# Performance work log

Hardware: AMD Instinct MI355X
Metric: run time of the kernel (lower is better)

## Reference

```python
import jax, jax.numpy as jnp
import numpy as np
from jax import lax

QMAX = 127.0  # symmetric int8 fake-quant levels
EPS = 1e-5    # batchnorm eps


def fq(x):
    """Per-tensor symmetric fake-quant with straight-through estimator.
    Simulates ChopSTE: round/clip to low precision in fwd, identity grad in bwd."""
    s = jnp.maximum(jnp.max(jnp.abs(x)) / QMAX, 1e-8)
    q = jnp.clip(jnp.round(x / s), -QMAX, QMAX) * s
    return x + lax.stop_gradient(q - x)


def conv2d(x, w, b):
    # NCHW input, OIHW kernel, padding=1 (SAME for 3x3)
    y = lax.conv_general_dilated(x, w, window_strides=(1, 1),
                                 padding=((1, 1), (1, 1)),
                                 dimension_numbers=('NCHW', 'OIHW', 'NCHW'))
    return y + b[None, :, None, None]


def maxpool2(x):
    return lax.reduce_window(x, -jnp.inf, lax.max, (1, 1, 2, 2), (1, 1, 2, 2), 'VALID')


def bn(x, g, be, m, v):
    inv = g / jnp.sqrt(v + EPS)  # [C]
    return x * inv[None, :, None, None] + (be - m * inv)[None, :, None, None]


def setup_inputs() -> dict:
    key = jax.random.key(0)
    ks = jax.random.split(key, 17)
    B = 8192
    d = {}
    d['x'] = jax.random.normal(ks[0], (B, 1, 28, 28), jnp.float32)
    d['w1'] = jax.random.normal(ks[1], (16, 1, 3, 3), jnp.float32) * 0.3
    d['b1'] = jax.random.normal(ks[2], (16,), jnp.float32) * 0.1
    d['g1'] = jax.random.uniform(ks[3], (16,), jnp.float32, 0.5, 1.5)
    d['be1'] = jax.random.normal(ks[4], (16,), jnp.float32) * 0.1
    d['m1'] = jax.random.normal(ks[5], (16,), jnp.float32) * 0.1
    d['v1'] = jax.random.uniform(ks[6], (16,), jnp.float32, 0.5, 1.5)
    d['w2'] = jax.random.normal(ks[7], (32, 16, 3, 3), jnp.float32) * 0.1
    d['b2'] = jax.random.normal(ks[8], (32,), jnp.float32) * 0.1
    d['g2'] = jax.random.uniform(ks[9], (32,), jnp.float32, 0.5, 1.5)
    d['be2'] = jax.random.normal(ks[10], (32,), jnp.float32) * 0.1
    d['m2'] = jax.random.normal(ks[11], (32,), jnp.float32) * 0.1
    d['v2'] = jax.random.uniform(ks[12], (32,), jnp.float32, 0.5, 1.5)
    d['fw1'] = jax.random.normal(ks[13], (128, 1568), jnp.float32) * 0.03
    d['fb1'] = jax.random.normal(ks[14], (128,), jnp.float32) * 0.1
    d['fw2'] = jax.random.normal(ks[15], (10, 128), jnp.float32) * 0.1
    d['fb2'] = jax.random.normal(ks[16], (10,), jnp.float32) * 0.1
    return d


def reference(x, w1, b1, g1, be1, m1, v1, w2, b2, g2, be2, m2, v2, fw1, fb1, fw2, fb2):
    # block 1: quantized conv -> quantized relu -> quantized bn -> maxpool
    h = fq(conv2d(x, fq(w1), b1))           # [B,16,28,28]
    h = fq(jax.nn.relu(h))
    h = fq(bn(h, g1, be1, m1, v1))
    h = maxpool2(h)                          # [B,16,14,14]
    # block 2
    h = fq(conv2d(h, fq(w2), b2))           # [B,32,14,14]
    h = fq(jax.nn.relu(h))
    h = fq(bn(h, g2, be2, m2, v2))
    h = maxpool2(h)                          # [B,32,7,7]
    # classifier (dropout is identity at inference)
    h = h.reshape(h.shape[0], -1)            # [B,1568]
    h = fq(h @ fq(fw1).T + fb1)              # [B,128]
    h = fq(jax.nn.relu(h))
    out = fq(h @ fq(fw2).T + fb2)            # [B,10]
    return out
```

## Files before the change

### kernel.cpp

```cpp
#include <hip/hip_runtime.h>
#include <math.h>
#include <limits.h>
#include <stdint.h>

#define QMAXF 127.0f
#define BN_EPS 1e-5f
#define NCOPIES 64

typedef int v4i __attribute__((ext_vector_type(4)));
typedef float f32x4 __attribute__((ext_vector_type(4)));
typedef _Float16 f16x8 __attribute__((ext_vector_type(8)));

__device__ __forceinline__ int f2ord(float f){
    int i = __float_as_int(f);
    return i ^ ((i >> 31) & 0x7fffffff);
}
__device__ __forceinline__ float ord2f(int i){
    return __int_as_float(i ^ ((i >> 31) & 0x7fffffff));
}
__device__ __forceinline__ float scale_from_ord(int om){
    return fmaxf(ord2f(om) / QMAXF, 1e-8f);
}
__device__ __forceinline__ float fq_apply(float x, float s){
    float q = rintf(x / s);
    q = fminf(fmaxf(q, -QMAXF), QMAXF);
    return q * s;
}
__device__ __forceinline__ float quant_k(float x, float s){
    float q = rintf(x / s);
    return fminf(fmaxf(q, -QMAXF), QMAXF);
}
__device__ __forceinline__ _Float16 hpart(uint32_t w){
    return __builtin_bit_cast(_Float16, (unsigned short)(w >> 16));
}
__device__ __forceinline__ _Float16 lpart(uint32_t w){
    return __builtin_bit_cast(_Float16, (unsigned short)(w & 0xffffu));
}

__global__ void k_init_stats(int* s1, int* s2, int* sf, int* so, int* wsmax){
    int t = blockIdx.x*blockDim.x + threadIdx.x;
    if (t < 2048){ int j = t & 31; s1[t] = (j < 16) ? INT_MAX : INT_MIN; }
    else if (t < 6144){ int u = t - 2048; int j = u & 63; s2[u] = (j < 32) ? INT_MAX : INT_MIN; }
    else if (t < 6272){ int u = t - 6144; sf[u] = ((u & 1) == 0) ? INT_MAX : INT_MIN; }
    else if (t < 6400){ int u = t - 6272; so[u] = ((u & 1) == 0) ? INT_MAX : INT_MIN; }
    else if (t < 6404){ wsmax[t - 6400] = INT_MIN; }
}

__global__ __launch_bounds__(256) void k_wscales(
    const float* __restrict__ w1, const float* __restrict__ w2,
    const float* __restrict__ fw1, const float* __restrict__ fw2,
    int* __restrict__ wsmax)
{
    __shared__ float red[256];
    int t = threadIdx.x, blk = blockIdx.x;
    const float* src; int n, base, which;
    if (blk < 64){ src = fw1; base = blk*3136; n = 3136; which = 2; }
    else if (blk == 64){ src = w1;  base = 0; n = 144;  which = 0; }
    else if (blk == 65){ src = w2;  base = 0; n = 4608; which = 1; }
    else { src = fw2; base = 0; n = 1280; which = 3; }
    float m = 0.f;
    for (int i = t; i < n; i += 256) m = fmaxf(m, fabsf(src[base + i]));
    red[t] = m; __syncthreads();
    for (int off = 128; off; off >>= 1){
        if (t < off) red[t] = fmaxf(red[t], red[t+off]);
        __syncthreads();
    }
    if (t == 0) atomicMax(&wsmax[which], f2ord(red[0]));
}

__global__ __launch_bounds__(256) void k_pack_weights(
    const float* __restrict__ w1, const float* __restrict__ w2,
    const float* __restrict__ fw1, const float* __restrict__ fw2,
    const int* __restrict__ wsmax,
    _Float16* __restrict__ wpk1h, int8_t* __restrict__ wpk2,
    int8_t* __restrict__ bpk1, float* __restrict__ qfw2,
    float* __restrict__ wscales)
{
    int blk = blockIdx.x, t = threadIdx.x;
    if (blk < 784){
        float s = scale_from_ord(wsmax[2]);
        int i = blk*256 + t;
        int o = i / 1568, k = i - o*1568;
        int c = k / 49, r = k - c*49;
        int kp = r*32 + c;
        int kchunk = kp >> 6, rem = kp & 63, hi = rem >> 4, j = rem & 15;
        int code = (int)quant_k(fw1[i], s);
        bpk1[(o>>4)*25600 + (kchunk*4 + hi)*256 + (o&15)*16 + j] = (int8_t)code;
    } else if (blk == 784){
        float s0 = scale_from_ord(wsmax[0]), s3 = scale_from_ord(wsmax[3]);
        for (int i = t; i < 512; i += 256){
            int grp = i >> 3, j = i & 7;
            int hi = grp >> 4, col = grp & 15;
            _Float16 val = (_Float16)0.f;
            if (hi < 3 && j < 3)
                val = (_Float16)quant_k(w1[col*9 + hi*3 + j], s0);
            wpk1h[i] = val;
        }
        for (int i = t; i < 1280; i += 256) qfw2[i] = fq_apply(fw2[i], s3);
        for (int i = t; i < 4096; i += 256){
            int o = i >> 5, rem = (i & 31) + 32;
            int hi = rem >> 4, j = rem & 15;
            bpk1[(o>>4)*25600 + (24*4 + hi)*256 + (o&15)*16 + j] = 0;
        }
        if (t < 4) wscales[t] = scale_from_ord(wsmax[t]);
    } else {
        float s1 = scale_from_ord(wsmax[1]);
        for (int i = t; i < 6144; i += 256) wpk2[i] = 0;
        __syncthreads();
        for (int i = t; i < 4608; i += 256){
            int co = i / 144, rr = i - co*144, ci = rr / 9, pix = rr - ci*9;
            wpk2[(co >> 4)*3072 + pix*256 + (co & 15)*16 + ci] = (int8_t)(int)quant_k(w2[i], s1);
        }
    }
}

__global__ __launch_bounds__(256) void k_prep_x(
    const float* __restrict__ x, uint32_t* __restrict__ xp)
{
    int i = blockIdx.x*256 + threadIdx.x;
    int b = i / 900, r = i - b*900;
    int yy = r / 30, xx = r - yy*30;
    float val = 0.f;
    if (yy >= 1 && yy <= 28 && xx >= 1 && xx <= 28)
        val = x[(size_t)b*784 + (yy-1)*28 + (xx-1)];
    _Float16 h  = (_Float16)val;
    _Float16 lo = (_Float16)(val - (float)h);
    xp[i] = ((uint32_t)__builtin_bit_cast(unsigned short, h) << 16)
          |  (uint32_t)__builtin_bit_cast(unsigned short, lo);
}

__device__ __forceinline__ void conv1_frag3(const uint32_t* __restrict__ base, bool valid,
                                            f16x8& ahi, f16x8& alo)
{
    uint32_t w0 = valid ? base[0] : 0u;
    uint32_t w1 = valid ? base[1] : 0u;
    uint32_t w2 = valid ? base[2] : 0u;
    _Float16 z = (_Float16)0.f;
    ahi = (f16x8){hpart(w0), hpart(w1), hpart(w2), z, z, z, z, z};
    alo = (f16x8){lpart(w0), lpart(w1), lpart(w2), z, z, z, z, z};
}

__global__ __launch_bounds__(256) void k_conv1s_mfma(
    const uint32_t* __restrict__ xp, const _Float16* __restrict__ wpk1h,
    const float* __restrict__ b1, const float* __restrict__ wscales,
    int* __restrict__ stats1)
{
    int t = threadIdx.x, l = t & 63, wid = t >> 6;
    int hi = l >> 4, col = l & 15;
    f16x8 bv = *(const f16x8*)(wpk1h + (hi*16 + col)*8);
    float sb = b1[col];
    float s0 = wscales[0];
    int tile0 = blockIdx.x*4 + wid;
    int p0 = tile0*16 + (l & 15);
    int b0 = p0 / 784, r = p0 - b0*784;
    int y = r / 28, xx = r - y*28;
    int rowo = (hi < 3) ? hi : 2;
    bool valid = hi < 3;
    const uint32_t* base = xp + (size_t)b0*900 + (y + rowo)*30 + xx;
    float mn = INFINITY, mx = -INFINITY;
    #pragma unroll 1
    for (int it = 0; it < 64; it++){
        f16x8 ahi, alo;
        conv1_frag3(base, valid, ahi, alo);
        f32x4 acc = {0.f, 0.f, 0.f, 0.f};
        acc = __builtin_amdgcn_mfma_f32_16x16x32_f16(ahi, bv, acc, 0, 0, 0);
        acc = __builtin_amdgcn_mfma_f32_16x16x32_f16(alo, bv, acc, 0, 0, 0);
        #pragma unroll
        for (int rg = 0; rg < 4; rg++){
            mn = fminf(mn, acc[rg]); mx = fmaxf(mx, acc[rg]);
        }
        base += (size_t)128*900;
    }
    mn = fmaf(s0, mn, sb);
    mx = fmaf(s0, mx, sb);
    mn = fminf(mn, __shfl_xor(mn, 16)); mn = fminf(mn, __shfl_xor(mn, 32));
    mx = fmaxf(mx, __shfl_xor(mx, 16)); mx = fmaxf(mx, __shfl_xor(mx, 32));
    if (l < 16){
        int* basep = stats1 + (blockIdx.x & (NCOPIES-1))*32;
        atomicMin(&basep[l],      f2ord(mn));
        atomicMax(&basep[16 + l], f2ord(mx));
    }
}

__global__ __launch_bounds__(256) void k_scales_block(
    const int* __restrict__ stats,
    const float* __restrict__ g, const float* __restrict__ be,
    const float* __restrict__ m, const float* __restrict__ v,
    float* __restrict__ s_out, int8_t* __restrict__ t1buf)
{
    __shared__ float cmn[16], cmx[16], invs[16], dds[16], sss[3];
    int t = threadIdx.x;
    if (t < 32){
        bool ismax = t >= 16; int c = t & 15;
        int acc = ismax ? INT_MIN : INT_MAX;
        for (int i = 0; i < NCOPIES; i++){
            int u = stats[i*32 + t];
            acc = ismax ? max(acc, u) : min(acc, u);
        }
        if (ismax) cmx[c] = ord2f(acc); else cmn[c] = ord2f(acc);
    }
    __syncthreads();
    if (t == 0){
        float am = 0.f;
        for (int c = 0; c < 16; c++) am = fmaxf(am, fmaxf(fabsf(cmn[c]), fabsf(cmx[c])));
        float sA_ = fmaxf(am / QMAXF, 1e-8f);
        float rmax = 0.f;
        float q1x[16], q1n[16];
        for (int c = 0; c < 16; c++){
            q1x[c] = fmaxf(fq_apply(cmx[c], sA_), 0.f);
            q1n[c] = fmaxf(fq_apply(cmn[c], sA_), 0.f);
            rmax = fmaxf(rmax, q1x[c]);
        }
        float sB_ = fmaxf(rmax / QMAXF, 1e-8f);
        float am3 = 0.f;
        for (int c = 0; c < 16; c++){
            float inv = g[c] / sqrtf(v[c] + BN_EPS);
            float dd  = be[c] - m[c]*inv;
            invs[c] = inv; dds[c] = dd;
            float ha = fmaf(fq_apply(q1x[c], sB_), inv, dd);
            float hb = fmaf(fq_apply(q1n[c], sB_), inv, dd);
            am3 = fmaxf(am3, fmaxf(fabsf(ha), fabsf(hb)));
        }
        float sC_ = fmaxf(am3 / QMAXF, 1e-8f);
        sss[0] = sA_; sss[1] = sB_; sss[2] = sC_;
        s_out[0] = sA_; s_out[1] = sB_; s_out[2] = sC_;
    }
    __syncthreads();
    float s1 = sss[0], s2 = sss[1], s3 = sss[2];
    for (int e = t; e < 2048; e += 256){
        int c = e >> 7, idx = e & 127;
        float hh = (float)idx * s1;
        float q2 = quant_k(hh, s2);
        float h2 = q2 * s2;
        float hb = fmaf(h2, invs[c], dds[c]);
        t1buf[e] = (int8_t)(int)quant_k(hb, s3);
    }
}

__global__ __launch_bounds__(256) void k_block1_mfma(
    const uint32_t* __restrict__ xp, const _Float16* __restrict__ wpk1h,
    const float* __restrict__ b1, const float* __restrict__ wscales,
    const float* __restrict__ scales, const int8_t* __restrict__ t1buf,
    int8_t* __restrict__ h1q)
{
    __shared__ int8_t T1l[16*132];
    int t = threadIdx.x, l = t & 63, wid = t >> 6;
    for (int e = t; e < 2048; e += 256)
        T1l[(e >> 7)*132 + (e & 127)] = t1buf[e];
    __syncthreads();
    int hi = l >> 4, col = l & 15;
    f16x8 bv = *(const f16x8*)(wpk1h + (hi*16 + col)*8);
    float sb = b1[col];
    float s0 = wscales[0], s1 = scales[0];
    int tile0 = blockIdx.x*4 + wid;
    int grow = tile0*16 + (l & 15);
    int cell = grow >> 2, sub = grow & 3;
    int b0 = cell / 196, rc = cell - b0*196;
    int py = rc / 14, px = rc - py*14;
    int y = 2*py + (sub >> 1), xx = 2*px + (sub & 1);
    int rowo = (hi < 3) ? hi : 2;
    bool valid = hi < 3;
    const uint32_t* base = xp + (size_t)b0*900 + (y + rowo)*30 + xx;
    const int8_t* T1c = T1l + col*132;
    int8_t* h1o = h1q + (size_t)tile0*64 + l;
    #pragma unroll 1
    for (int it = 0; it < 16; it++){
        f16x8 ahi, alo;
        conv1_frag3(base, valid, ahi, alo);
        f32x4 acc = {0.f, 0.f, 0.f, 0.f};
        acc = __builtin_amdgcn_mfma_f32_16x16x32_f16(ahi, bv, acc, 0, 0, 0);
        acc = __builtin_amdgcn_mfma_f32_16x16x32_f16(alo, bv, acc, 0, 0, 0);
        float pool = fmaxf(fmaxf(acc[0], acc[1]), fmaxf(acc[2], acc[3]));
        float conv = fmaf(s0, pool, sb);
        float q = quant_k(conv, s1);
        int idx = (int)fmaxf(q, 0.f);
        *h1o = T1c[idx];
        base += (size_t)512*900;
        h1o  += (size_t)100352*16;
    }
}

__global__ __launch_bounds__(256) void k_conv2s_mfma(
    const int8_t* __restrict__ h1q, const int8_t* __restrict__ wpk2,
    int* __restrict__ stats2)
{
    __shared__ int smn[32], smx[32];
    int t = threadIdx.x, l = t & 63, wid = t >> 6;
    if (t < 32){ smn[t] = INT_MAX; smx[t] = INT_MIN; }
    __syncthreads();
    int hi = l >> 4;
    v4i bv[6];
    #pragma unroll
    for (int nt = 0; nt < 2; nt++)
        #pragma unroll
        for (int s = 0; s < 3; s++)
            bv[nt*3+s] = *(const v4i*)(wpk2 + nt*3072 + (4*s + hi)*256 + (l&15)*16);
    int tile0 = blockIdx.x*4 + wid;
    int grow = tile0*16 + (l & 15);
    int cell_g = grow >> 2;
    int b0 = cell_g / 49, cell = cell_g - b0*49;
    int sub = grow & 3;
    int qy = cell / 7, qx = cell - qy*7;
    int y = 2*qy + (sub >> 1), x = 2*qx + (sub & 1);
    const int8_t* ip = h1q + (size_t)b0*196*16;
    int toff[3];
    #pragma unroll
    for (int s = 0; s < 3; s++){
        int tap = 4*s + hi;
        toff[s] = -1;
        if (tap < 9){
            int ky = tap / 3, kx = tap - ky*3;
            int yy = y + ky - 1, xc = x + kx - 1;
            if (yy >= 0 && yy < 14 && xc >= 0 && xc < 14)
                toff[s] = (yy*14 + xc)*16;
        }
    }
    int mn0 = INT_MAX, mx0 = INT_MIN, mn1 = INT_MAX, mx1 = INT_MIN;
    #pragma unroll 1
    for (int it = 0; it < 16; it++){
        v4i acc0 = (v4i){0,0,0,0}, acc1 = (v4i){0,0,0,0};
        #pragma unroll
        for (int s = 0; s < 3; s++){
            v4i av = (toff[s] >= 0) ? *(const v4i*)(ip + toff[s]) : (v4i){0,0,0,0};
            acc0 = __builtin_amdgcn_mfma_i32_16x16x64_i8(av, bv[s],     acc0, 0, 0, 0);
            acc1 = __builtin_amdgcn_mfma_i32_16x16x64_i8(av, bv[3 + s], acc1, 0, 0, 0);
        }
        #pragma unroll
        for (int r = 0; r < 4; r++){
            mn0 = min(mn0, acc0[r]); mx0 = max(mx0, acc0[r]);
            mn1 = min(mn1, acc1[r]); mx1 = max(mx1, acc1[r]);
        }
        ip += (size_t)512*196*16;
    }
    mn0 = min(mn0, __shfl_xor(mn0, 16)); mn0 = min(mn0, __shfl_xor(mn0, 32));
    mx0 = max(mx0, __shfl_xor(mx0, 16)); mx0 = max(mx0, __shfl_xor(mx0, 32));
    mn1 = min(mn1, __shfl_xor(mn1, 16)); mn1 = min(mn1, __shfl_xor(mn1, 32));
    mx1 = max(mx1, __shfl_xor(mx1, 16)); mx1 = max(mx1, __shfl_xor(mx1, 32));
    if (l < 16){
        atomicMin(&smn[l], mn0);      atomicMax(&smx[l], mx0);
        atomicMin(&smn[16 + l], mn1); atomicMax(&smx[16 + l], mx1);
    }
    __syncthreads();
    if (t < 32){
        int* basep = stats2 + (blockIdx.x & (NCOPIES-1))*64;
        atomicMin(&basep[t],      smn[t]);
        atomicMax(&basep[t + 32], smx[t]);
    }
}

__global__ __launch_bounds__(256) void k_scales2(
    const int* __restrict__ stats,
    const float* __restrict__ g, const float* __restrict__ be,
    const float* __restrict__ m, const float* __restrict__ v,
    const float* __restrict__ b2,
    const float* __restrict__ scales, const float* __restrict__ wscales,
    float* __restrict__ s_out, int8_t* __restrict__ t2buf)
{
    __shared__ float cmn[32], cmx[32], invs[32], dds[32], sss[3];
    int t = threadIdx.x;
    float S = scales[2] * wscales[1];
    if (t < 64){
        bool ismax = t >= 32; int c = t & 31;
        int acc = ismax ? INT_MIN : INT_MAX;
        for (int i = 0; i < NCOPIES; i++){
            int u = stats[i*64 + t];
            acc = ismax ? max(acc, u) : min(acc, u);
        }
        float val = fmaf(S, (float)acc, b2[c]);
        if (ismax) cmx[c] = val; else cmn[c] = val;
    }
    __syncthreads();
    if (t == 0){
        float am = 0.f;
        for (int c = 0; c < 32; c++) am = fmaxf(am, fmaxf(fabsf(cmn[c]), fabsf(cmx[c])));
        float sA_ = fmaxf(am / QMAXF, 1e-8f);
        float rmax = 0.f;
        float q1x[32], q1n[32];
        for (int c = 0; c < 32; c++){
            q1x[c] = fmaxf(fq_apply(cmx[c], sA_), 0.f);
            q1n[c] = fmaxf(fq_apply(cmn[c], sA_), 0.f);
            rmax = fmaxf(rmax, q1x[c]);
        }
        float sB_ = fmaxf(rmax / QMAXF, 1e-8f);
        float am3 = 0.f;
        for (int c = 0; c < 32; c++){
            float inv = g[c] / sqrtf(v[c] + BN_EPS);
            float dd  = be[c] - m[c]*inv;
            invs[c] = inv; dds[c] = dd;
            float ha = fmaf(fq_apply(q1x[c], sB_), inv, dd);
            float hb = fmaf(fq_apply(q1n[c], sB_), inv, dd);
            am3 = fmaxf(am3, fmaxf(fabsf(ha), fabsf(hb)));
        }
        float sC_ = fmaxf(am3 / QMAXF, 1e-8f);
        sss[0] = sA_; sss[1] = sB_; sss[2] = sC_;
        s_out[0] = sA_; s_out[1] = sB_; s_out[2] = sC_;
    }
    __syncthreads();
    float s4 = sss[0], s5 = sss[1], s6 = sss[2];
    for (int e = t; e < 4096; e += 256){
        int c = e >> 7, idx = e & 127;
        float hh = (float)idx * s4;
        float q5 = quant_k(hh, s5);
        float h2 = q5 * s5;
        float hb = fmaf(h2, invs[c], dds[c]);
        t2buf[e] = (int8_t)(int)quant_k(hb, s6);
    }
}

__global__ __launch_bounds__(256) void k_block2_mfma(
    const int8_t* __restrict__ h1q, const int8_t* __restrict__ wpk2,
    const float* __restrict__ b2, const float* __restrict__ scales,
    const float* __restrict__ wscales, const int8_t* __restrict__ t2buf,
    int8_t* __restrict__ h2q)
{
    __shared__ int8_t T2l[32*132];
    int t = threadIdx.x, l = t & 63, wid = t >> 6;
    for (int e = t; e < 4096; e += 256)
        T2l[(e >> 7)*132 + (e & 127)] = t2buf[e];
    __syncthreads();
    int hi = l >> 4, cl = l & 15;
    float S = scales[2] * wscales[1];
    float s4 = scales[3];
    float sb0 = b2[cl], sb1 = b2[16 + cl];
    const int8_t* T2a = T2l + cl*132;
    const int8_t* T2b = T2l + (16 + cl)*132;
    v4i bv[6];
    #pragma unroll
    for (int nt = 0; nt < 2; nt++)
        #pragma unroll
        for (int s = 0; s < 3; s++)
            bv[nt*3+s] = *(const v4i*)(wpk2 + nt*3072 + (4*s + hi)*256 + cl*16);
    int tile0 = blockIdx.x*4 + wid;
    int grow = tile0*16 + (l & 15);
    int cell_g = grow >> 2;
    int b0 = cell_g / 49, cell = cell_g - b0*49;
    int sub = grow & 3;
    int qy = cell / 7, qx = cell - qy*7;
    int y = 2*qy + (sub >> 1), x = 2*qx + (sub & 1);
    const int8_t* ip = h1q + (size_t)b0*196*16;
    int toff[3];
    #pragma unroll
    for (int s = 0; s < 3; s++){
        int tap = 4*s + hi;
        toff[s] = -1;
        if (tap < 9){
            int ky = tap / 3, kx = tap - ky*3;
            int yy = y + ky - 1, xc = x + kx - 1;
            if (yy >= 0 && yy < 14 && xc >= 0 && xc < 14)
                toff[s] = (yy*14 + xc)*16;
        }
    }
    int8_t* h2o = h2q + (size_t)(tile0*4 + hi)*32 + cl;
    #pragma unroll 1
    for (int it = 0; it < 4; it++){
        v4i acc0 = (v4i){0,0,0,0}, acc1 = (v4i){0,0,0,0};
        #pragma unroll
        for (int s = 0; s < 3; s++){
            v4i av = (toff[s] >= 0) ? *(const v4i*)(ip + toff[s]) : (v4i){0,0,0,0};
            acc0 = __builtin_amdgcn_mfma_i32_16x16x64_i8(av, bv[s],     acc0, 0, 0, 0);
            acc1 = __builtin_amdgcn_mfma_i32_16x16x64_i8(av, bv[3 + s], acc1, 0, 0, 0);
        }
        int pool0 = max(max(acc0[0], acc0[1]), max(acc0[2], acc0[3]));
        int pool1 = max(max(acc1[0], acc1[1]), max(acc1[2], acc1[3]));
        float q0 = quant_k(fmaf(S, (float)pool0, sb0), s4);
        float q1 = quant_k(fmaf(S, (float)pool1, sb1), s4);
        h2o[0]  = T2a[(int)fmaxf(q0, 0.f)];
        h2o[16] = T2b[(int)fmaxf(q1, 0.f)];
        ip  += (size_t)2048*196*16;
        h2o += (size_t)100352*32;
    }
}

__global__ __launch_bounds__(256) void k_fc1(
    const int8_t* __restrict__ h2q, const int8_t* __restrict__ bpk1,
    const float* __restrict__ fb1, const float* __restrict__ scales,
    const float* __restrict__ wscales,
    float* __restrict__ fc1o, int* __restrict__ statsFc)
{
    __shared__ int smn, smx;
    int t = threadIdx.x, l = t & 63, wid = t >> 6;
    if (t == 0){ smn = INT_MAX; smx = INT_MIN; }
    __syncthreads();
    int wave_id = blockIdx.x*4 + wid;
    int mtile = wave_id >> 2;
    int quarter = wave_id & 3;
    int hi = l >> 4, lo = l & 15;
    const int8_t* arow = h2q + (size_t)(mtile*16 + lo)*1568;
    v4i acc[2];
    #pragma unroll
    for (int g = 0; g < 2; g++) acc[g] = (v4i){0,0,0,0};
    #pragma unroll 1
    for (int kc = 0; kc < 25; kc++){
        int koff = kc*64 + hi*16;
        v4i av = (v4i){0,0,0,0};
        if (koff < 1568) av = *(const v4i*)(arow + koff);
        #pragma unroll
        for (int g = 0; g < 2; g++){
            v4i bvv = *(const v4i*)(bpk1 + (quarter*2 + g)*25600 + (kc*4 + hi)*256 + lo*16);
            acc[g] = __builtin_amdgcn_mfma_i32_16x16x64_i8(av, bvv, acc[g], 0, 0, 0);
        }
    }
    float Sfc = scales[5] * wscales[2];
    float lmn = INFINITY, lmx = -INFINITY;
    #pragma unroll
    for (int g = 0; g < 2; g++){
        int o = (quarter*2 + g)*16 + lo;
        float bias = fb1[o];
        #pragma unroll
        for (int r = 0; r < 4; r++){
            int m = mtile*16 + hi*4 + r;
            float val = fmaf(Sfc, (float)acc[g][r], bias);
            fc1o[(size_t)m*128 + o] = val;
            lmn = fminf(lmn, val); lmx = fmaxf(lmx, val);
        }
    }
    #pragma unroll
    for (int d = 1; d < 64; d <<= 1){
        lmn = fminf(lmn, __shfl_xor(lmn, d));
        lmx = fmaxf(lmx, __shfl_xor(lmx, d));
    }
    if (l == 0){
        atomicMin(&smn, f2ord(lmn));
        atomicMax(&smx, f2ord(lmx));
    }
    __syncthreads();
    if (t == 0){
        int* basep = statsFc + (blockIdx.x & (NCOPIES-1))*2;
        atomicMin(&basep[0], smn); atomicMax(&basep[1], smx);
    }
}

__global__ __launch_bounds__(256) void k_fc2(
    const float* __restrict__ fc1o, const float* __restrict__ qfw2, const float* __restrict__ fb2,
    const int* __restrict__ statsFc, float* __restrict__ out, int* __restrict__ statsOut)
{
    __shared__ float sw[1280], sb2[10], Tf[128];
    __shared__ float s7sh, s8sh;
    __shared__ int smn, smx;
    int t = threadIdx.x;
    for (int i = t; i < 1280; i += 256) sw[i] = qfw2[i];
    if (t < 10) sb2[t] = fb2[t];
    if (t == 0){
        smn = INT_MAX; smx = INT_MIN;
        int mni = INT_MAX, mxi = INT_MIN;
        for (int i = 0; i < NCOPIES; i++){ mni = min(mni, statsFc[i*2]); mxi = max(mxi, statsFc[i*2+1]); }
        float mn = ord2f(mni), mx = ord2f(mxi);
        float am = fmaxf(fabsf(mn), fabsf(mx));
        float s7 = fmaxf(am / QMAXF, 1e-8f);
        float rmx = fmaxf(fq_apply(mx, s7), 0.f);
        s7sh = s7; s8sh = fmaxf(rmx / QMAXF, 1e-8f);
    }
    __syncthreads();
    float s7 = s7sh, s8 = s8sh;
    if (t < 128) Tf[t] = s8 * quant_k((float)t * s7, s8);
    __syncthreads();
    int b = blockIdx.x*256 + t;
    float acc[10];
    #pragma unroll
    for (int j = 0; j < 10; j++) acc[j] = sb2[j];
    const float* fp = fc1o + (size_t)b*128;
    for (int k = 0; k < 128; k += 4){
        float4 f = *(const float4*)(fp + k);
        float v0 = Tf[(int)fmaxf(quant_k(f.x, s7), 0.f)];
        float v1 = Tf[(int)fmaxf(quant_k(f.y, s7), 0.f)];
        float v2 = Tf[(int)fmaxf(quant_k(f.z, s7), 0.f)];
        float v3 = Tf[(int)fmaxf(quant_k(f.w, s7), 0.f)];
        #pragma unroll
        for (int j = 0; j < 10; j++){
            float a = acc[j];
            a = fmaf(v0, sw[j*128 + k],     a);
            a = fmaf(v1, sw[j*128 + k + 1], a);
            a = fmaf(v2, sw[j*128 + k + 2], a);
            a = fmaf(v3, sw[j*128 + k + 3], a);
            acc[j] = a;
        }
    }
    float lmn = INFINITY, lmx = -INFINITY;
    #pragma unroll
    for (int j = 0; j < 10; j++){
        out[(size_t)b*10 + j] = acc[j];
        lmn = fminf(lmn, acc[j]); lmx = fmaxf(lmx, acc[j]);
    }
    atomicMin(&smn, f2ord(lmn)); atomicMax(&smx, f2ord(lmx));
    __syncthreads();
    if (t == 0){
        int* basep = statsOut + (blockIdx.x & (NCOPIES-1))*2;
        atomicMin(&basep[0], smn); atomicMax(&basep[1], smx);
    }
}

__global__ void k_quant_out(float* __restrict__ out, const int* __restrict__ statsOut, int n){
    __shared__ float s9s;
    if (threadIdx.x == 0){
        int mni = INT_MAX, mxi = INT_MIN;
        for (int i = 0; i < NCOPIES; i++){ mni = min(mni, statsOut[i*2]); mxi = max(mxi, statsOut[i*2+1]); }
        float am = fmaxf(fabsf(ord2f(mni)), fabsf(ord2f(mxi)));
        s9s = fmaxf(am / QMAXF, 1e-8f);
    }
    __syncthreads();
    int i = blockIdx.x*256 + threadIdx.x;
    if (i < n) out[i] = fq_apply(out[i], s9s);
}

extern "C" void kernel_launch(void* const* d_in, const int* in_sizes, int n_in,
                              void* d_out, int out_size, void* d_ws, size_t ws_size,
                              hipStream_t stream)
{
    const float* x   = (const float*)d_in[0];
    const float* w1  = (const float*)d_in[1];
    const float* b1  = (const float*)d_in[2];
    const float* g1  = (const float*)d_in[3];
    const float* be1 = (const float*)d_in[4];
    const float* m1  = (const float*)d_in[5];
    const float* v1  = (const float*)d_in[6];
    const float* w2  = (const float*)d_in[7];
    const float* b2  = (const float*)d_in[8];
    const float* g2  = (const float*)d_in[9];
    const float* be2 = (const float*)d_in[10];
    const float* m2  = (const float*)d_in[11];
    const float* v2  = (const float*)d_in[12];
    const float* fw1 = (const float*)d_in[13];
    const float* fb1 = (const float*)d_in[14];
    const float* fw2 = (const float*)d_in[15];
    const float* fb2 = (const float*)d_in[16];
    float* out = (float*)d_out;

    char* ws = (char*)d_ws;
    size_t off = 0;
    auto alloc = [&](size_t bytes)->char*{
        char* p = ws + off;
        off = (off + bytes + 255) & ~(size_t)255;
        return p;
    };
    _Float16* wpk1h = (_Float16*)alloc(512*2);
    int8_t* wpk2  = (int8_t*)alloc(6144);
    int8_t* bpk1  = (int8_t*)alloc(204800);
    float* qfw2   = (float*)alloc(1280*4);
    float* scales = (float*)alloc(16*4);
    float* wscales= (float*)alloc(4*4);
    int* wsmax    = (int*)alloc(4*4);
    int8_t* t1buf = (int8_t*)alloc(2048);
    int8_t* t2buf = (int8_t*)alloc(4096);
    int* stats1   = (int*)alloc(64*32*4);
    int* stats2   = (int*)alloc(64*64*4);
    int* statsFc  = (int*)alloc(64*2*4);
    int* statsOut = (int*)alloc(64*2*4);
    uint32_t* xp  = (uint32_t*)alloc((size_t)8192*900*4);
    int8_t* h1q   = (int8_t*)alloc((size_t)8192*196*16);
    int8_t* h2q   = (int8_t*)alloc((size_t)8192*49*32);
    float* fc1o   = (float*)alloc((size_t)8192*128*4);
    (void)ws_size;

    k_init_stats<<<26, 256, 0, stream>>>(stats1, stats2, statsFc, statsOut, wsmax);
    k_wscales<<<67, 256, 0, stream>>>(w1, w2, fw1, fw2, wsmax);
    k_pack_weights<<<786, 256, 0, stream>>>(w1, w2, fw1, fw2, wsmax, wpk1h, wpk2, bpk1, qfw2, wscales);
    k_prep_x<<<28800, 256, 0, stream>>>(x, xp);
    k_conv1s_mfma<<<1568, 256, 0, stream>>>(xp, wpk1h, b1, wscales, stats1);
    k_scales_block<<<1, 256, 0, stream>>>(stats1, g1, be1, m1, v1, scales + 0, t1buf);
    k_block1_mfma<<<6272, 256, 0, stream>>>(xp, wpk1h, b1, wscales, scales, t1buf, h1q);
    k_conv2s_mfma<<<1568, 256, 0, stream>>>(h1q, wpk2, stats2);
    k_scales2<<<1, 256, 0, stream>>>(stats2, g2, be2, m2, v2, b2, scales, wscales, scales + 3, t2buf);
    k_block2_mfma<<<6272, 256, 0, stream>>>(h1q, wpk2, b2, scales, wscales, t2buf, h2q);
    k_fc1<<<512, 256, 0, stream>>>(h2q, bpk1, fb1, scales, wscales, fc1o, statsFc);
    k_fc2<<<32, 256, 0, stream>>>(fc1o, qfw2, fb2, statsFc, out, statsOut);
    k_quant_out<<<320, 256, 0, stream>>>(out, statsOut, out_size);
}
```

Measured before the change: 216.4 us.

## Pack fp16 hi/lo split into one MFMA and merge setup kernels

The conv1 A-fragment now carries the high and low fp16 halves of each input in separate k slots, and the packed weights are duplicated to match. A single MFMA then replaces two, and each iteration processes two independent tiles. The weight abs-max step writes per-block partials instead of using atomics, and the init, wscales, pack and input-prep kernels are merged into two launches. The trade-off is that every fw1 pack thread re-reduces 64 partials, and the merged kernel mixes heterogeneous block types.

```diff
diff --git a/kernel.cpp b/kernel.cpp
--- a/kernel.cpp
+++ b/kernel.cpp
@@ -18,8 +18,8 @@
 __device__ __forceinline__ float ord2f(int i){
     return __int_as_float(i ^ ((i >> 31) & 0x7fffffff));
 }
-__device__ __forceinline__ float scale_from_ord(int om){
-    return fmaxf(ord2f(om) / QMAXF, 1e-8f);
+__device__ __forceinline__ float scale_of(float m){
+    return fmaxf(m / QMAXF, 1e-8f);
 }
 __device__ __forceinline__ float fq_apply(float x, float s){
     float q = rintf(x / s);
@@ -37,27 +37,28 @@
     return __builtin_bit_cast(_Float16, (unsigned short)(w & 0xffffu));
 }
 
-__global__ void k_init_stats(int* s1, int* s2, int* sf, int* so, int* wsmax){
-    int t = blockIdx.x*blockDim.x + threadIdx.x;
-    if (t < 2048){ int j = t & 31; s1[t] = (j < 16) ? INT_MAX : INT_MIN; }
-    else if (t < 6144){ int u = t - 2048; int j = u & 63; s2[u] = (j < 32) ? INT_MAX : INT_MIN; }
-    else if (t < 6272){ int u = t - 6144; sf[u] = ((u & 1) == 0) ? INT_MAX : INT_MIN; }
-    else if (t < 6400){ int u = t - 6272; so[u] = ((u & 1) == 0) ? INT_MAX : INT_MIN; }
-    else if (t < 6404){ wsmax[t - 6400] = INT_MIN; }
-}
-
-__global__ __launch_bounds__(256) void k_wscales(
+__global__ __launch_bounds__(256) void k_init_ws(
     const float* __restrict__ w1, const float* __restrict__ w2,
     const float* __restrict__ fw1, const float* __restrict__ fw2,
-    int* __restrict__ wsmax)
-{
+    int* __restrict__ s1, int* __restrict__ s2, int* __restrict__ sf, int* __restrict__ so,
+    float* __restrict__ wsbuf )
+{
+    int blk = blockIdx.x, t = threadIdx.x;
+    if (blk < 26){
+        int gt = blk*256 + t;
+        if (gt < 2048){ int j = gt & 31; s1[gt] = (j < 16) ? INT_MAX : INT_MIN; }
+        else if (gt < 6144){ int u = gt - 2048; int j = u & 63; s2[u] = (j < 32) ? INT_MAX : INT_MIN; }
+        else if (gt < 6272){ int u = gt - 6144; sf[u] = ((u & 1) == 0) ? INT_MAX : INT_MIN; }
+        else if (gt < 6400){ int u = gt - 6272; so[u] = ((u & 1) == 0) ? INT_MAX : INT_MIN; }
+        return;
+    }
     __shared__ float red[256];
-    int t = threadIdx.x, blk = blockIdx.x;
-    const float* src; int n, base, which;
-    if (blk < 64){ src = fw1; base = blk*3136; n = 3136; which = 2; }
-    else if (blk == 64){ src = w1;  base = 0; n = 144;  which = 0; }
-    else if (blk == 65){ src = w2;  base = 0; n = 4608; which = 1; }
-    else { src = fw2; base = 0; n = 1280; which = 3; }
+    int b2 = blk - 26;
+    const float* src; int n, base;
+    if (b2 < 64){ src = fw1; base = b2*3136; n = 3136; }
+    else if (b2 == 64){ src = w1;  base = 0; n = 144; }
+    else if (b2 == 65){ src = w2;  base = 0; n = 4608; }
+    else { src = fw2; base = 0; n = 1280; }
     float m = 0.f;
     for (int i = t; i < n; i += 256) m = fmaxf(m, fabsf(src[base + i]));
     red[t] = m; __syncthreads();
@@ -65,20 +66,37 @@
         if (t < off) red[t] = fmaxf(red[t], red[t+off]);
         __syncthreads();
     }
-    if (t == 0) atomicMax(&wsmax[which], f2ord(red[0]));
-}
-
-__global__ __launch_bounds__(256) void k_pack_weights(
+    if (t == 0) wsbuf[b2] = red[0];
+}
+
+__global__ __launch_bounds__(256) void k_pack_prep(
+    const float* __restrict__ x,
     const float* __restrict__ w1, const float* __restrict__ w2,
     const float* __restrict__ fw1, const float* __restrict__ fw2,
-    const int* __restrict__ wsmax,
+    const float* __restrict__ wsbuf,
     _Float16* __restrict__ wpk1h, int8_t* __restrict__ wpk2,
     int8_t* __restrict__ bpk1, float* __restrict__ qfw2,
-    float* __restrict__ wscales)
+    float* __restrict__ wscales, uint32_t* __restrict__ xp)
 {
     int blk = blockIdx.x, t = threadIdx.x;
+    if (blk >= 786){
+        int i = (blk - 786)*256 + t;
+        int b = i / 900, r = i - b*900;
+        int yy = r / 30, xx = r - yy*30;
+        float val = 0.f;
+        if (yy >= 1 && yy <= 28 && xx >= 1 && xx <= 28)
+            val = x[(size_t)b*784 + (yy-1)*28 + (xx-1)];
+        _Float16 h  = (_Float16)val;
+        _Float16 lo = (_Float16)(val - (float)h);
+        xp[i] = ((uint32_t)__builtin_bit_cast(unsigned short, h) << 16)
+              |  (uint32_t)__builtin_bit_cast(unsigned short, lo);
+        return;
+    }
     if (blk < 784){
-        float s = scale_from_ord(wsmax[2]);
+        float m = 0.f;
+        #pragma unroll
+        for (int i = 0; i < 64; i++) m = fmaxf(m, wsbuf[i]);
+        float s = scale_of(m);
         int i = blk*256 + t;
         int o = i / 1568, k = i - o*1568;
         int c = k / 49, r = k - c*49;
@@ -87,13 +105,15 @@
         int code = (int)quant_k(fw1[i], s);
         bpk1[(o>>4)*25600 + (kchunk*4 + hi)*256 + (o&15)*16 + j] = (int8_t)code;
     } else if (blk == 784){
-        float s0 = scale_from_ord(wsmax[0]), s3 = scale_from_ord(wsmax[3]);
+        float s0 = scale_of(wsbuf[64]), s3 = scale_of(wsbuf[66]);
         for (int i = t; i < 512; i += 256){
             int grp = i >> 3, j = i & 7;
             int hi = grp >> 4, col = grp & 15;
             _Float16 val = (_Float16)0.f;
-            if (hi < 3 && j < 3)
-                val = (_Float16)quant_k(w1[col*9 + hi*3 + j], s0);
+            if (hi < 3){
+                int jj = (j < 3) ? j : ((j < 6) ? (j - 3) : -1);
+                if (jj >= 0) val = (_Float16)quant_k(w1[col*9 + hi*3 + jj], s0);
+            }
             wpk1h[i] = val;
         }
         for (int i = t; i < 1280; i += 256) qfw2[i] = fq_apply(fw2[i], s3);
@@ -102,9 +122,16 @@
             int hi = rem >> 4, j = rem & 15;
             bpk1[(o>>4)*25600 + (24*4 + hi)*256 + (o&15)*16 + j] = 0;
         }
-        if (t < 4) wscales[t] = scale_from_ord(wsmax[t]);
+        if (t == 0){
+            float m = 0.f;
+            for (int i = 0; i < 64; i++) m = fmaxf(m, wsbuf[i]);
+            wscales[0] = scale_of(wsbuf[64]);
+            wscales[1] = scale_of(wsbuf[65]);
+            wscales[2] = scale_of(m);
+            wscales[3] = scale_of(wsbuf[66]);
+        }
     } else {
-        float s1 = scale_from_ord(wsmax[1]);
+        float s1 = scale_of(wsbuf[65]);
         for (int i = t; i < 6144; i += 256) wpk2[i] = 0;
         __syncthreads();
         for (int i = t; i < 4608; i += 256){
@@ -114,30 +141,14 @@
     }
 }
 
-__global__ __launch_bounds__(256) void k_prep_x(
-    const float* __restrict__ x, uint32_t* __restrict__ xp)
-{
-    int i = blockIdx.x*256 + threadIdx.x;
-    int b = i / 900, r = i - b*900;
-    int yy = r / 30, xx = r - yy*30;
-    float val = 0.f;
-    if (yy >= 1 && yy <= 28 && xx >= 1 && xx <= 28)
-        val = x[(size_t)b*784 + (yy-1)*28 + (xx-1)];
-    _Float16 h  = (_Float16)val;
-    _Float16 lo = (_Float16)(val - (float)h);
-    xp[i] = ((uint32_t)__builtin_bit_cast(unsigned short, h) << 16)
-          |  (uint32_t)__builtin_bit_cast(unsigned short, lo);
-}
-
-__device__ __forceinline__ void conv1_frag3(const uint32_t* __restrict__ base, bool valid,
-                                            f16x8& ahi, f16x8& alo)
+__device__ __forceinline__ f16x8 conv1_fragHL(const uint32_t* __restrict__ base, bool valid)
 {
     uint32_t w0 = valid ? base[0] : 0u;
     uint32_t w1 = valid ? base[1] : 0u;
     uint32_t w2 = valid ? base[2] : 0u;
     _Float16 z = (_Float16)0.f;
-    ahi = (f16x8){hpart(w0), hpart(w1), hpart(w2), z, z, z, z, z};
-    alo = (f16x8){lpart(w0), lpart(w1), lpart(w2), z, z, z, z, z};
+    return (f16x8){hpart(w0), hpart(w1), hpart(w2),
+                   lpart(w0), lpart(w1), lpart(w2), z, z};
 }
 
 __global__ __launch_bounds__(256) void k_conv1s_mfma(
@@ -159,17 +170,19 @@
     const uint32_t* base = xp + (size_t)b0*900 + (y + rowo)*30 + xx;
     float mn = INFINITY, mx = -INFINITY;
     #pragma unroll 1
-    for (int it = 0; it < 64; it++){
-        f16x8 ahi, alo;
-        conv1_frag3(base, valid, ahi, alo);
-        f32x4 acc = {0.f, 0.f, 0.f, 0.f};
-        acc = __builtin_amdgcn_mfma_f32_16x16x32_f16(ahi, bv, acc, 0, 0, 0);
-        acc = __builtin_amdgcn_mfma_f32_16x16x32_f16(alo, bv, acc, 0, 0, 0);
+    for (int it = 0; it < 32; it++){
+        const uint32_t* base2 = base + (size_t)128*900;
+        f16x8 a0 = conv1_fragHL(base,  valid);
+        f16x8 a1 = conv1_fragHL(base2, valid);
+        f32x4 c0 = {0.f,0.f,0.f,0.f}, c1 = {0.f,0.f,0.f,0.f};
+        c0 = __builtin_amdgcn_mfma_f32_16x16x32_f16(a0, bv, c0, 0, 0, 0);
+        c1 = __builtin_amdgcn_mfma_f32_16x16x32_f16(a1, bv, c1, 0, 0, 0);
         #pragma unroll
         for (int rg = 0; rg < 4; rg++){
-            mn = fminf(mn, acc[rg]); mx = fmaxf(mx, acc[rg]);
-        }
-        base += (size_t)128*900;
+            mn = fminf(mn, fminf(c0[rg], c1[rg]));
+            mx = fmaxf(mx, fmaxf(c0[rg], c1[rg]));
+        }
+        base += (size_t)256*900;
     }
     mn = fmaf(s0, mn, sb);
     mx = fmaf(s0, mx, sb);
@@ -264,19 +277,21 @@
     const int8_t* T1c = T1l + col*132;
     int8_t* h1o = h1q + (size_t)tile0*64 + l;
     #pragma unroll 1
-    for (int it = 0; it < 16; it++){
-        f16x8 ahi, alo;
-        conv1_frag3(base, valid, ahi, alo);
-        f32x4 acc = {0.f, 0.f, 0.f, 0.f};
-        acc = __builtin_amdgcn_mfma_f32_16x16x32_f16(ahi, bv, acc, 0, 0, 0);
-        acc = __builtin_amdgcn_mfma_f32_16x16x32_f16(alo, bv, acc, 0, 0, 0);
-        float pool = fmaxf(fmaxf(acc[0], acc[1]), fmaxf(acc[2], acc[3]));
-        float conv = fmaf(s0, pool, sb);
-        float q = quant_k(conv, s1);
-        int idx = (int)fmaxf(q, 0.f);
-        *h1o = T1c[idx];
-        base += (size_t)512*900;
-        h1o  += (size_t)100352*16;
+    for (int it = 0; it < 8; it++){
+        const uint32_t* base2 = base + (size_t)512*900;
+        f16x8 a0 = conv1_fragHL(base,  valid);
+        f16x8 a1 = conv1_fragHL(base2, valid);
+        f32x4 c0 = {0.f,0.f,0.f,0.f}, c1 = {0.f,0.f,0.f,0.f};
+        c0 = __builtin_amdgcn_mfma_f32_16x16x32_f16(a0, bv, c0, 0, 0, 0);
+        c1 = __builtin_amdgcn_mfma_f32_16x16x32_f16(a1, bv, c1, 0, 0, 0);
+        float pool0 = fmaxf(fmaxf(c0[0], c0[1]), fmaxf(c0[2], c0[3]));
+        float pool1 = fmaxf(fmaxf(c1[0], c1[1]), fmaxf(c1[2], c1[3]));
+        float q0 = quant_k(fmaf(s0, pool0, sb), s1);
+        float q1 = quant_k(fmaf(s0, pool1, sb), s1);
+        h1o[0]                  = T1c[(int)fmaxf(q0, 0.f)];
+        h1o[(size_t)100352*16]  = T1c[(int)fmaxf(q1, 0.f)];
+        base += (size_t)1024*900;
+        h1o  += (size_t)2*100352*16;
     }
 }
 
@@ -638,7 +653,7 @@
     float* qfw2   = (float*)alloc(1280*4);
     float* scales = (float*)alloc(16*4);
     float* wscales= (float*)alloc(4*4);
-    int* wsmax    = (int*)alloc(4*4);
+    float* wsbuf  = (float*)alloc(67*4);
     int8_t* t1buf = (int8_t*)alloc(2048);
     int8_t* t2buf = (int8_t*)alloc(4096);
     int* stats1   = (int*)alloc(64*32*4);
@@ -651,10 +666,8 @@
     float* fc1o   = (float*)alloc((size_t)8192*128*4);
     (void)ws_size;
 
-    k_init_stats<<<26, 256, 0, stream>>>(stats1, stats2, statsFc, statsOut, wsmax);
-    k_wscales<<<67, 256, 0, stream>>>(w1, w2, fw1, fw2, wsmax);
-    k_pack_weights<<<786, 256, 0, stream>>>(w1, w2, fw1, fw2, wsmax, wpk1h, wpk2, bpk1, qfw2, wscales);
-    k_prep_x<<<28800, 256, 0, stream>>>(x, xp);
+    k_init_ws<<<93, 256, 0, stream>>>(w1, w2, fw1, fw2, stats1, stats2, statsFc, statsOut, wsbuf);
+    k_pack_prep<<<29586, 256, 0, stream>>>(x, w1, w2, fw1, fw2, wsbuf, wpk1h, wpk2, bpk1, qfw2, wscales, xp);
     k_conv1s_mfma<<<1568, 256, 0, stream>>>(xp, wpk1h, b1, wscales, stats1);
     k_scales_block<<<1, 256, 0, stream>>>(stats1, g1, be1, m1, v1, scales + 0, t1buf);
     k_block1_mfma<<<6272, 256, 0, stream>>>(xp, wpk1h, b1, wscales, scales, t1buf, h1q);
```

Measured after the change: 197.8 us. -8.6%, faster.
